# Kernel tuning notes

Measured on AMD Instinct MI355X. Metric: run time of the kernel, lower is better.

## Reference

```python
import jax, jax.numpy as jnp
import numpy as np
from math import comb

N_SEG = 100000      # number of Bezier segments
BEZ_ORDER = 3       # cubic Bezier -> 4 control points per segment
D = 3               # point dimension
BATCH, NPTS = 8, 1000000


def setup_inputs() -> dict:
    key = jax.random.key(0)
    k1, k2, k3 = jax.random.split(key, 3)
    # strictly ascending knot vector: cumsum of positive dx, starting at 0
    dx = jax.random.uniform(k1, (N_SEG,), dtype=jnp.float32, minval=0.5, maxval=1.5)
    x_knots = jnp.concatenate([jnp.zeros((1,), jnp.float32), jnp.cumsum(dx)])
    x_end = x_knots[-1]
    # eval points spread beyond [0, x_end) so the modulo wrap is exercised
    x_eval = jax.random.uniform(k2, (BATCH, NPTS), dtype=jnp.float32) * (2.0 * x_end) - 0.5 * x_end
    control_points = jax.random.normal(k3, (N_SEG, BEZ_ORDER + 1, D), dtype=jnp.float32)
    return {"x_knots": x_knots, "control_points": control_points, "x_eval": x_eval}


def _bernstein_basis(s, n):
    # s: [N] in [0,1] -> basis [N, n+1]; powers via cumprod (differentiable at s=0/1)
    binom = jnp.asarray([comb(n, k) for k in range(n + 1)], dtype=s.dtype)
    t = s[:, None]
    ones = jnp.ones_like(t)
    t_pow = jnp.cumprod(jnp.concatenate([ones, jnp.broadcast_to(t, (t.shape[0], n))], axis=1), axis=1)         # t^k
    u = 1.0 - t
    u_pow = jnp.cumprod(jnp.concatenate([ones, jnp.broadcast_to(u, (u.shape[0], n))], axis=1), axis=1)         # u^k
    return binom * t_pow * u_pow[:, ::-1]  # C(n,k) t^k (1-t)^(n-k)


def reference(x_knots, control_points, x_eval):
    n = control_points.shape[1] - 1
    d = control_points.shape[2]
    xstart = x_knots[:-1]                      # [n_seg]
    dx = x_knots[1:] - x_knots[:-1]            # [n_seg]
    # x_true = x_eval % xend  (Python modulo semantics, matches torch %)
    x_true = jnp.mod(x_eval.reshape(-1), x_knots[-1])        # [N]
    # bucket search: segment index such that xstart[i] <= x_true < xstart[i+1]
    idx = jnp.clip(jnp.searchsorted(xstart, x_true, side='right') - 1, 0, xstart.shape[0] - 1)
    s = (x_true - xstart[idx]) / dx[idx]                     # local param in [0,1)
    basis = _bernstein_basis(s, n)                           # [N, n+1]
    P = control_points[idx]                                  # gather: [N, n+1, d]
    vals = jnp.einsum('nk,nkd->nd', basis, P)                # [N, d]
    return vals.reshape(x_eval.shape + (d,)), idx.reshape(x_eval.shape)
```

## Files before the change

### kernel.cpp

```cpp
#include <hip/hip_runtime.h>
#include <hip/hip_fp16.h>
#include <math.h>

#define N_SEG 100000
#define LUT_BITS 18
#define LUT_SIZE (1 << LUT_BITS)
#define DELTA 0.03
#define PPT 4

using f32x4 = __attribute__((ext_vector_type(4))) float;
using u32x4 = __attribute__((ext_vector_type(4))) unsigned int;

#define LUT_OFF 0
#define REC_OFF (1 << 20)
#define WS_NEED (REC_OFF + (size_t)(N_SEG + 1) * 32)

__device__ __forceinline__ unsigned packh(float lo, float hi) {
    unsigned a = (unsigned)__half_as_ushort(__float2half(lo));
    unsigned b = (unsigned)__half_as_ushort(__float2half(hi));
    return a | (b << 16);
}
__device__ __forceinline__ float h2f(unsigned w, int hi) {
    return __half2float(__ushort_as_half((unsigned short)(hi ? (w >> 16) : (w & 0xFFFFu))));
}

__device__ __forceinline__ float mod_reduce(float x, float xe) {
    float r = x;
    r = (x >= xe) ? (x - xe) : r;
    r = (x < 0.0f) ? (x + xe) : r;
    return r;
}

__global__ void __launch_bounds__(256)
build_lut_kernel(const float* __restrict__ xk, unsigned* __restrict__ lut4) {
    int j = blockIdx.x * blockDim.x + threadIdx.x;
    if (j >= LUT_SIZE) return;
    double Wd = (double)xk[N_SEG] / (double)LUT_SIZE;
    double t = (double)j * Wd - DELTA;
    int lo = 0, hi = N_SEG;
    while (lo < hi) {
        int mid = (lo + hi) >> 1;
        if ((double)xk[mid] <= t) lo = mid + 1; else hi = mid;
    }
    int base = lo - 1;
    base = base < 0 ? 0 : (base > N_SEG - 1 ? N_SEG - 1 : base);
    lut4[j] = (unsigned)base;
}

__global__ void __launch_bounds__(256)
build_rec_kernel(const float* __restrict__ xk, const float* __restrict__ cp,
                 u32x4* __restrict__ rec) {
    int i = blockIdx.x * blockDim.x + threadIdx.x;
    if (i > N_SEG) return;
    if (i == N_SEG) {
        u32x4 w0 = { __float_as_uint(xk[N_SEG]), __float_as_uint(xk[N_SEG] + 1.0f), 0u, 0u };
        u32x4 w1 = { 0u, 0u, 0u, 0u };
        rec[2 * (size_t)i] = w0;
        rec[2 * (size_t)i + 1] = w1;
        return;
    }
    float x0 = xk[i];
    float x1 = xk[i + 1];
    const f32x4* p = reinterpret_cast<const f32x4*>(cp + (size_t)i * 12);
    f32x4 a0 = p[0], a1 = p[1], a2 = p[2];
    u32x4 w0 = { __float_as_uint(x0), __float_as_uint(x1),
                 packh(a0.x, a0.y), packh(a0.z, a0.w) };
    u32x4 w1 = { packh(a1.x, a1.y), packh(a1.z, a1.w),
                 packh(a2.x, a2.y), packh(a2.z, a2.w) };
    rec[2 * (size_t)i]     = w0;
    rec[2 * (size_t)i + 1] = w1;
}

__device__ __forceinline__ void blend_from_words(
        float r, int base, u32x4 A0, u32x4 A1, u32x4 B0, u32x4 B1,
        float* v, float* idxf) {
    float x0a = __uint_as_float(A0.x);
    float x1a = __uint_as_float(A0.y);
    int c = ((x1a <= r) && (base < N_SEG - 1)) ? 1 : 0;
    float x0 = c ? x1a : x0a;
    float x1 = c ? __uint_as_float(B0.y) : x1a;
    float s  = (r - x0) / (x1 - x0);

    unsigned cw0 = c ? B0.z : A0.z;
    unsigned cw1 = c ? B0.w : A0.w;
    unsigned cw2 = c ? B1.x : A1.x;
    unsigned cw3 = c ? B1.y : A1.y;
    unsigned cw4 = c ? B1.z : A1.z;
    unsigned cw5 = c ? B1.w : A1.w;

    float u = 1.0f - s;
    float s2 = s * s, u2 = u * u;
    float b0 = u2 * u;
    float b1 = (3.0f * s) * u2;
    float b2 = (3.0f * s2) * u;
    float b3 = s2 * s;

    float c0 = h2f(cw0, 0), c1  = h2f(cw0, 1);
    float c2 = h2f(cw1, 0), c3  = h2f(cw1, 1);
    float c4 = h2f(cw2, 0), c5  = h2f(cw2, 1);
    float c6 = h2f(cw3, 0), c7  = h2f(cw3, 1);
    float c8 = h2f(cw4, 0), c9  = h2f(cw4, 1);
    float c10 = h2f(cw5, 0), c11 = h2f(cw5, 1);

    v[0] = b0 * c0 + b1 * c3 + b2 * c6 + b3 * c9;
    v[1] = b0 * c1 + b1 * c4 + b2 * c7 + b3 * c10;
    v[2] = b0 * c2 + b1 * c5 + b2 * c8 + b3 * c11;
    *idxf = (float)(base + c);
}

__global__ void __launch_bounds__(256)
eval_kernel(const float* __restrict__ xk,
            const float* __restrict__ xev,
            float* __restrict__ out_vals,
            float* __restrict__ out_idx,
            const unsigned char* __restrict__ ws,
            int npts) {
    __shared__ u32x4 stage[4 * PPT * 4 * 64];
    unsigned char* stg = reinterpret_cast<unsigned char*>(stage);
    const unsigned* lut4 = reinterpret_cast<const unsigned*>(ws + LUT_OFF);
    const unsigned char* rec = ws + REC_OFF;

    int t = blockIdx.x * blockDim.x + threadIdx.x;
    int lane = threadIdx.x & 63;
    int wave = threadIdx.x >> 6;
    unsigned wbase = (unsigned)wave * (PPT * 4 * 1024);
    long i0 = (long)t * PPT;

    float xe = xk[N_SEG];
    float invW = (float)LUT_SIZE / xe;

    if (i0 + PPT - 1 < (long)npts) {
        f32x4 x4 = __builtin_nontemporal_load(reinterpret_cast<const f32x4*>(xev) + t);
        float r[PPT] = {x4.x, x4.y, x4.z, x4.w};
        #pragma unroll
        for (int q = 0; q < PPT; ++q) {
            r[q] = mod_reduce(r[q], xe);
            int j = (int)(r[q] * invW);
            j = j < 0 ? 0 : (j > LUT_SIZE - 1 ? LUT_SIZE - 1 : j);
            __builtin_amdgcn_global_load_lds(
                (const __attribute__((address_space(1))) void*)(lut4 + j),
                (__attribute__((address_space(3))) void*)(stg + wbase + q * 256 + lane * 4),
                4, 0, 0);
        }
        asm volatile("s_waitcnt vmcnt(0)" ::: "memory");
        __builtin_amdgcn_sched_barrier(0);

        int base[PPT];
        #pragma unroll
        for (int q = 0; q < PPT; ++q) {
            base[q] = *reinterpret_cast<volatile int*>(stg + wbase + q * 256 + lane * 4);
        }
        asm volatile("s_waitcnt lgkmcnt(0)" ::: "memory");
        __builtin_amdgcn_sched_barrier(0);

        #pragma unroll
        for (int q = 0; q < PPT; ++q) {
            const unsigned char* w = rec + (size_t)base[q] * 32;
            #pragma unroll
            for (int k = 0; k < 4; ++k) {
                __builtin_amdgcn_global_load_lds(
                    (const __attribute__((address_space(1))) void*)(w + 16 * k),
                    (__attribute__((address_space(3))) void*)(stg + wbase + (q * 4 + k) * 1024 + lane * 16),
                    16, 0, 0);
            }
        }
        asm volatile("s_waitcnt vmcnt(0)" ::: "memory");
        __builtin_amdgcn_sched_barrier(0);

        float vals[PPT * 3];
        float idxf[PPT];
        #pragma unroll
        for (int q = 0; q < PPT; ++q) {
            const u32x4* pl = reinterpret_cast<const u32x4*>(stg + wbase + q * 4096 + lane * 16);
            u32x4 A0 = pl[0];
            u32x4 A1 = pl[64];
            u32x4 B0 = pl[128];
            u32x4 B1 = pl[192];
            blend_from_words(r[q], base[q], A0, A1, B0, B1, &vals[q * 3], &idxf[q]);
        }
        f32x4* ov = reinterpret_cast<f32x4*>(out_vals + (size_t)t * 12);
        #pragma unroll
        for (int q = 0; q < 3; ++q) {
            f32x4 o = {vals[4 * q], vals[4 * q + 1], vals[4 * q + 2], vals[4 * q + 3]};
            ov[q] = o;
        }
        f32x4 oi = {idxf[0], idxf[1], idxf[2], idxf[3]};
        reinterpret_cast<f32x4*>(out_idx)[t] = oi;
    } else {
        for (long i = i0; i < (long)npts && i < i0 + PPT; ++i) {
            float r = mod_reduce(xev[i], xe);
            int j = (int)(r * invW);
            j = j < 0 ? 0 : (j > LUT_SIZE - 1 ? LUT_SIZE - 1 : j);
            int base = (int)lut4[j];
            const u32x4* w = reinterpret_cast<const u32x4*>(rec + (size_t)base * 32);
            u32x4 A0 = w[0], A1 = w[1], B0 = w[2], B1 = w[3];
            float v[3], idxv;
            blend_from_words(r, base, A0, A1, B0, B1, v, &idxv);
            out_vals[(size_t)i * 3 + 0] = v[0];
            out_vals[(size_t)i * 3 + 1] = v[1];
            out_vals[(size_t)i * 3 + 2] = v[2];
            out_idx[i] = idxv;
        }
    }
}

__global__ void __launch_bounds__(256)
eval_kernel_bs(const float* __restrict__ xk,
               const float* __restrict__ cp,
               const float* __restrict__ xev,
               float* __restrict__ out_vals,
               float* __restrict__ out_idx,
               int npts) {
    int i = blockIdx.x * blockDim.x + threadIdx.x;
    if (i >= npts) return;
    float xe = xk[N_SEG];
    float r = mod_reduce(xev[i], xe);
    int lo = 0, hi = N_SEG;
    while (lo < hi) {
        int mid = (lo + hi) >> 1;
        if (xk[mid] <= r) lo = mid + 1; else hi = mid;
    }
    int idx = lo - 1;
    if (idx < 0) idx = 0;
    float x0 = xk[idx];
    float s = (r - x0) / (xk[idx + 1] - x0);
    float u = 1.0f - s;
    float s2 = s * s, u2 = u * u;
    float b0 = u2 * u, b1f = (3.0f * s) * u2, b2f = (3.0f * s2) * u, b3f = s2 * s;
    const f32x4* p = reinterpret_cast<const f32x4*>(cp + (size_t)idx * 12);
    f32x4 pA = p[0], pB = p[1], pC = p[2];
    out_vals[(size_t)i * 3 + 0] = b0 * pA.x + b1f * pA.w + b2f * pB.z + b3f * pC.y;
    out_vals[(size_t)i * 3 + 1] = b0 * pA.y + b1f * pB.x + b2f * pB.w + b3f * pC.z;
    out_vals[(size_t)i * 3 + 2] = b0 * pA.z + b1f * pB.y + b2f * pC.x + b3f * pC.w;
    out_idx[i] = (float)idx;
}

extern "C" void kernel_launch(void* const* d_in, const int* in_sizes, int n_in,
                              void* d_out, int out_size, void* d_ws, size_t ws_size,
                              hipStream_t stream) {
    const float* xk  = (const float*)d_in[0];
    const float* cp  = (const float*)d_in[1];
    const float* xev = (const float*)d_in[2];
    int npts = in_sizes[2];

    float* out_vals = (float*)d_out;
    float* out_idx  = out_vals + (size_t)npts * 3;

    if (ws_size >= WS_NEED) {
        unsigned char* ws = (unsigned char*)d_ws;
        unsigned* lut4 = (unsigned*)(ws + LUT_OFF);
        u32x4*   rec   = (u32x4*)(ws + REC_OFF);
        build_lut_kernel<<<(LUT_SIZE + 255) / 256, 256, 0, stream>>>(xk, lut4);
        build_rec_kernel<<<(N_SEG + 1 + 255) / 256, 256, 0, stream>>>(xk, cp, rec);
        long nthreads = ((long)npts + PPT - 1) / PPT;
        int nblocks = (int)((nthreads + 255) / 256);
        eval_kernel<<<nblocks, 256, 0, stream>>>(xk, xev, out_vals, out_idx, ws, npts);
    } else {
        int nblocks = (npts + 255) / 256;
        eval_kernel_bs<<<nblocks, 256, 0, stream>>>(xk, cp, xev, out_vals, out_idx, npts);
    }
}
```

Before: 172.7 us.

## Store next-knot boundary in LUT entry to resolve segment before record fetch

Each LUT entry now holds the base segment plus the next knot position (8 bytes instead of 4). The kernel picks the exact segment from the LUT before fetching the record, so it loads only one 32-byte record per point instead of two. The LUT load also becomes a plain register load rather than an LDS-staged one. This halves the dependent gather traffic and the LDS staging footprint, at the cost of a LUT twice as large.

```diff
diff --git a/kernel.cpp b/kernel.cpp
--- a/kernel.cpp
+++ b/kernel.cpp
@@ -12,8 +12,8 @@
 using u32x4 = __attribute__((ext_vector_type(4))) unsigned int;
 
 #define LUT_OFF 0
-#define REC_OFF (1 << 20)
-#define WS_NEED (REC_OFF + (size_t)(N_SEG + 1) * 32)
+#define REC_OFF (2 << 20)
+#define WS_NEED (REC_OFF + (size_t)N_SEG * 32)
 
 __device__ __forceinline__ unsigned packh(float lo, float hi) {
     unsigned a = (unsigned)__half_as_ushort(__float2half(lo));
@@ -32,7 +32,7 @@
 }
 
 __global__ void __launch_bounds__(256)
-build_lut_kernel(const float* __restrict__ xk, unsigned* __restrict__ lut4) {
+build_lut_kernel(const float* __restrict__ xk, int2* __restrict__ lut8) {
     int j = blockIdx.x * blockDim.x + threadIdx.x;
     if (j >= LUT_SIZE) return;
     double Wd = (double)xk[N_SEG] / (double)LUT_SIZE;
@@ -44,21 +44,18 @@
     }
     int base = lo - 1;
     base = base < 0 ? 0 : (base > N_SEG - 1 ? N_SEG - 1 : base);
-    lut4[j] = (unsigned)base;
+    int2 e;
+    e.x = base;
+    e.y = (base + 1 <= N_SEG - 1) ? __float_as_int(xk[base + 1])
+                                  : __float_as_int(__builtin_inff());
+    lut8[j] = e;
 }
 
 __global__ void __launch_bounds__(256)
 build_rec_kernel(const float* __restrict__ xk, const float* __restrict__ cp,
                  u32x4* __restrict__ rec) {
     int i = blockIdx.x * blockDim.x + threadIdx.x;
-    if (i > N_SEG) return;
-    if (i == N_SEG) {
-        u32x4 w0 = { __float_as_uint(xk[N_SEG]), __float_as_uint(xk[N_SEG] + 1.0f), 0u, 0u };
-        u32x4 w1 = { 0u, 0u, 0u, 0u };
-        rec[2 * (size_t)i] = w0;
-        rec[2 * (size_t)i + 1] = w1;
-        return;
-    }
+    if (i >= N_SEG) return;
     float x0 = xk[i];
     float x1 = xk[i + 1];
     const f32x4* p = reinterpret_cast<const f32x4*>(cp + (size_t)i * 12);
@@ -71,22 +68,11 @@
     rec[2 * (size_t)i + 1] = w1;
 }
 
-__device__ __forceinline__ void blend_from_words(
-        float r, int base, u32x4 A0, u32x4 A1, u32x4 B0, u32x4 B1,
-        float* v, float* idxf) {
-    float x0a = __uint_as_float(A0.x);
-    float x1a = __uint_as_float(A0.y);
-    int c = ((x1a <= r) && (base < N_SEG - 1)) ? 1 : 0;
-    float x0 = c ? x1a : x0a;
-    float x1 = c ? __uint_as_float(B0.y) : x1a;
+__device__ __forceinline__ void blend_sel(float r, u32x4 A0, u32x4 A1,
+                                          float* v) {
+    float x0 = __uint_as_float(A0.x);
+    float x1 = __uint_as_float(A0.y);
     float s  = (r - x0) / (x1 - x0);
-
-    unsigned cw0 = c ? B0.z : A0.z;
-    unsigned cw1 = c ? B0.w : A0.w;
-    unsigned cw2 = c ? B1.x : A1.x;
-    unsigned cw3 = c ? B1.y : A1.y;
-    unsigned cw4 = c ? B1.z : A1.z;
-    unsigned cw5 = c ? B1.w : A1.w;
 
     float u = 1.0f - s;
     float s2 = s * s, u2 = u * u;
@@ -95,17 +81,16 @@
     float b2 = (3.0f * s2) * u;
     float b3 = s2 * s;
 
-    float c0 = h2f(cw0, 0), c1  = h2f(cw0, 1);
-    float c2 = h2f(cw1, 0), c3  = h2f(cw1, 1);
-    float c4 = h2f(cw2, 0), c5  = h2f(cw2, 1);
-    float c6 = h2f(cw3, 0), c7  = h2f(cw3, 1);
-    float c8 = h2f(cw4, 0), c9  = h2f(cw4, 1);
-    float c10 = h2f(cw5, 0), c11 = h2f(cw5, 1);
+    float c0 = h2f(A0.z, 0), c1  = h2f(A0.z, 1);
+    float c2 = h2f(A0.w, 0), c3  = h2f(A0.w, 1);
+    float c4 = h2f(A1.x, 0), c5  = h2f(A1.x, 1);
+    float c6 = h2f(A1.y, 0), c7  = h2f(A1.y, 1);
+    float c8 = h2f(A1.z, 0), c9  = h2f(A1.z, 1);
+    float c10 = h2f(A1.w, 0), c11 = h2f(A1.w, 1);
 
     v[0] = b0 * c0 + b1 * c3 + b2 * c6 + b3 * c9;
     v[1] = b0 * c1 + b1 * c4 + b2 * c7 + b3 * c10;
     v[2] = b0 * c2 + b1 * c5 + b2 * c8 + b3 * c11;
-    *idxf = (float)(base + c);
 }
 
 __global__ void __launch_bounds__(256)
@@ -115,15 +100,15 @@
             float* __restrict__ out_idx,
             const unsigned char* __restrict__ ws,
             int npts) {
-    __shared__ u32x4 stage[4 * PPT * 4 * 64];
+    __shared__ u32x4 stage[4 * PPT * 2 * 64];
     unsigned char* stg = reinterpret_cast<unsigned char*>(stage);
-    const unsigned* lut4 = reinterpret_cast<const unsigned*>(ws + LUT_OFF);
+    const int2* lut8 = reinterpret_cast<const int2*>(ws + LUT_OFF);
     const unsigned char* rec = ws + REC_OFF;
 
     int t = blockIdx.x * blockDim.x + threadIdx.x;
     int lane = threadIdx.x & 63;
     int wave = threadIdx.x >> 6;
-    unsigned wbase = (unsigned)wave * (PPT * 4 * 1024);
+    unsigned wbase = (unsigned)wave * (PPT * 2 * 1024);
     long i0 = (long)t * PPT;
 
     float xe = xk[N_SEG];
@@ -132,51 +117,42 @@
     if (i0 + PPT - 1 < (long)npts) {
         f32x4 x4 = __builtin_nontemporal_load(reinterpret_cast<const f32x4*>(xev) + t);
         float r[PPT] = {x4.x, x4.y, x4.z, x4.w};
+
+        int2 e[PPT];
         #pragma unroll
         for (int q = 0; q < PPT; ++q) {
             r[q] = mod_reduce(r[q], xe);
             int j = (int)(r[q] * invW);
             j = j < 0 ? 0 : (j > LUT_SIZE - 1 ? LUT_SIZE - 1 : j);
-            __builtin_amdgcn_global_load_lds(
-                (const __attribute__((address_space(1))) void*)(lut4 + j),
-                (__attribute__((address_space(3))) void*)(stg + wbase + q * 256 + lane * 4),
-                4, 0, 0);
+            e[q] = lut8[j];
+        }
+        __builtin_amdgcn_sched_barrier(0);
+
+        int idx[PPT];
+        #pragma unroll
+        for (int q = 0; q < PPT; ++q) {
+            idx[q] = e[q].x + ((__int_as_float(e[q].y) <= r[q]) ? 1 : 0);
+            const unsigned char* w = rec + (size_t)idx[q] * 32;
+            #pragma unroll
+            for (int k = 0; k < 2; ++k) {
+                __builtin_amdgcn_global_load_lds(
+                    (const __attribute__((address_space(1))) void*)(w + 16 * k),
+                    (__attribute__((address_space(3))) void*)(stg + wbase + (q * 2 + k) * 1024 + lane * 16),
+                    16, 0, 0);
+            }
         }
         asm volatile("s_waitcnt vmcnt(0)" ::: "memory");
         __builtin_amdgcn_sched_barrier(0);
 
-        int base[PPT];
-        #pragma unroll
-        for (int q = 0; q < PPT; ++q) {
-            base[q] = *reinterpret_cast<volatile int*>(stg + wbase + q * 256 + lane * 4);
-        }
-        asm volatile("s_waitcnt lgkmcnt(0)" ::: "memory");
-        __builtin_amdgcn_sched_barrier(0);
-
-        #pragma unroll
-        for (int q = 0; q < PPT; ++q) {
-            const unsigned char* w = rec + (size_t)base[q] * 32;
-            #pragma unroll
-            for (int k = 0; k < 4; ++k) {
-                __builtin_amdgcn_global_load_lds(
-                    (const __attribute__((address_space(1))) void*)(w + 16 * k),
-                    (__attribute__((address_space(3))) void*)(stg + wbase + (q * 4 + k) * 1024 + lane * 16),
-                    16, 0, 0);
-            }
-        }
-        asm volatile("s_waitcnt vmcnt(0)" ::: "memory");
-        __builtin_amdgcn_sched_barrier(0);
-
         float vals[PPT * 3];
         float idxf[PPT];
         #pragma unroll
         for (int q = 0; q < PPT; ++q) {
-            const u32x4* pl = reinterpret_cast<const u32x4*>(stg + wbase + q * 4096 + lane * 16);
+            const u32x4* pl = reinterpret_cast<const u32x4*>(stg + wbase + q * 2048 + lane * 16);
             u32x4 A0 = pl[0];
             u32x4 A1 = pl[64];
-            u32x4 B0 = pl[128];
-            u32x4 B1 = pl[192];
-            blend_from_words(r[q], base[q], A0, A1, B0, B1, &vals[q * 3], &idxf[q]);
+            blend_sel(r[q], A0, A1, &vals[q * 3]);
+            idxf[q] = (float)idx[q];
         }
         f32x4* ov = reinterpret_cast<f32x4*>(out_vals + (size_t)t * 12);
         #pragma unroll
@@ -191,15 +167,16 @@
             float r = mod_reduce(xev[i], xe);
             int j = (int)(r * invW);
             j = j < 0 ? 0 : (j > LUT_SIZE - 1 ? LUT_SIZE - 1 : j);
-            int base = (int)lut4[j];
-            const u32x4* w = reinterpret_cast<const u32x4*>(rec + (size_t)base * 32);
-            u32x4 A0 = w[0], A1 = w[1], B0 = w[2], B1 = w[3];
-            float v[3], idxv;
-            blend_from_words(r, base, A0, A1, B0, B1, v, &idxv);
+            int2 e = lut8[j];
+            int idx = e.x + ((__int_as_float(e.y) <= r) ? 1 : 0);
+            const u32x4* w = reinterpret_cast<const u32x4*>(rec + (size_t)idx * 32);
+            u32x4 A0 = w[0], A1 = w[1];
+            float v[3];
+            blend_sel(r, A0, A1, v);
             out_vals[(size_t)i * 3 + 0] = v[0];
             out_vals[(size_t)i * 3 + 1] = v[1];
             out_vals[(size_t)i * 3 + 2] = v[2];
-            out_idx[i] = idxv;
+            out_idx[i] = (float)idx;
         }
     }
 }
@@ -248,10 +225,10 @@
 
     if (ws_size >= WS_NEED) {
         unsigned char* ws = (unsigned char*)d_ws;
-        unsigned* lut4 = (unsigned*)(ws + LUT_OFF);
-        u32x4*   rec   = (u32x4*)(ws + REC_OFF);
-        build_lut_kernel<<<(LUT_SIZE + 255) / 256, 256, 0, stream>>>(xk, lut4);
-        build_rec_kernel<<<(N_SEG + 1 + 255) / 256, 256, 0, stream>>>(xk, cp, rec);
+        int2*  lut8 = (int2*)(ws + LUT_OFF);
+        u32x4* rec  = (u32x4*)(ws + REC_OFF);
+        build_lut_kernel<<<(LUT_SIZE + 255) / 256, 256, 0, stream>>>(xk, lut8);
+        build_rec_kernel<<<(N_SEG + 255) / 256, 256, 0, stream>>>(xk, cp, rec);
         long nthreads = ((long)npts + PPT - 1) / PPT;
         int nblocks = (int)((nthreads + 255) / 256);
         eval_kernel<<<nblocks, 256, 0, stream>>>(xk, xev, out_vals, out_idx, ws, npts);
```

New measurement: 161.0 us. 1.07x faster.

## Replace LDS-staged gathers with register gathers and double points per thread

Applied to the files above, without the earlier changes.

Removes the global_load_lds staging through shared memory for the LUT lookup and record gathers. The gathers now load straight into VGPRs, with asm pins and sched barriers keeping all loads issued before any use. Points per thread go from 4 to 8 to raise memory-level parallelism, and launch bounds ask for 4 blocks per CU. The cost is higher VGPR pressure (32 u32x4 values held in flight), which could cut occupancy or cause spills. The grid launch must also shrink to match PPT, and that part of the host code is not shown.

```diff
diff --git a/kernel.cpp b/kernel.cpp
--- a/kernel.cpp
+++ b/kernel.cpp
@@ -6,7 +6,7 @@
 #define LUT_BITS 18
 #define LUT_SIZE (1 << LUT_BITS)
 #define DELTA 0.03
-#define PPT 4
+#define PPT 8
 
 using f32x4 = __attribute__((ext_vector_type(4))) float;
 using u32x4 = __attribute__((ext_vector_type(4))) unsigned int;
@@ -14,6 +14,8 @@
 #define LUT_OFF 0
 #define REC_OFF (1 << 20)
 #define WS_NEED (REC_OFF + (size_t)(N_SEG + 1) * 32)
+
+#define PIN(x) asm volatile("" :: "v"(x))
 
 __device__ __forceinline__ unsigned packh(float lo, float hi) {
     unsigned a = (unsigned)__half_as_ushort(__float2half(lo));
@@ -55,7 +57,7 @@
     if (i == N_SEG) {
         u32x4 w0 = { __float_as_uint(xk[N_SEG]), __float_as_uint(xk[N_SEG] + 1.0f), 0u, 0u };
         u32x4 w1 = { 0u, 0u, 0u, 0u };
-        rec[2 * (size_t)i] = w0;
+        rec[2 * (size_t)i]     = w0;
         rec[2 * (size_t)i + 1] = w1;
         return;
     }
@@ -71,9 +73,9 @@
     rec[2 * (size_t)i + 1] = w1;
 }
 
-__device__ __forceinline__ void blend_from_words(
-        float r, int base, u32x4 A0, u32x4 A1, u32x4 B0, u32x4 B1,
-        float* v, float* idxf) {
+__device__ __forceinline__ void blend_window(float r, int base,
+                                             u32x4 A0, u32x4 A1, u32x4 B0, u32x4 B1,
+                                             float* v, float* idxf) {
     float x0a = __uint_as_float(A0.x);
     float x1a = __uint_as_float(A0.y);
     int c = ((x1a <= r) && (base < N_SEG - 1)) ? 1 : 0;
@@ -108,94 +110,83 @@
     *idxf = (float)(base + c);
 }
 
-__global__ void __launch_bounds__(256)
+__global__ void __launch_bounds__(256, 4)
 eval_kernel(const float* __restrict__ xk,
             const float* __restrict__ xev,
             float* __restrict__ out_vals,
             float* __restrict__ out_idx,
             const unsigned char* __restrict__ ws,
             int npts) {
-    __shared__ u32x4 stage[4 * PPT * 4 * 64];
-    unsigned char* stg = reinterpret_cast<unsigned char*>(stage);
     const unsigned* lut4 = reinterpret_cast<const unsigned*>(ws + LUT_OFF);
-    const unsigned char* rec = ws + REC_OFF;
+    const u32x4* rec = reinterpret_cast<const u32x4*>(ws + REC_OFF);
 
     int t = blockIdx.x * blockDim.x + threadIdx.x;
-    int lane = threadIdx.x & 63;
-    int wave = threadIdx.x >> 6;
-    unsigned wbase = (unsigned)wave * (PPT * 4 * 1024);
     long i0 = (long)t * PPT;
 
     float xe = xk[N_SEG];
     float invW = (float)LUT_SIZE / xe;
 
     if (i0 + PPT - 1 < (long)npts) {
-        f32x4 x4 = __builtin_nontemporal_load(reinterpret_cast<const f32x4*>(xev) + t);
-        float r[PPT] = {x4.x, x4.y, x4.z, x4.w};
+        f32x4 xa = __builtin_nontemporal_load(reinterpret_cast<const f32x4*>(xev) + 2 * t);
+        f32x4 xb = __builtin_nontemporal_load(reinterpret_cast<const f32x4*>(xev) + 2 * t + 1);
+        float r[PPT] = {xa.x, xa.y, xa.z, xa.w, xb.x, xb.y, xb.z, xb.w};
+        const unsigned* lp[PPT];
         #pragma unroll
         for (int q = 0; q < PPT; ++q) {
             r[q] = mod_reduce(r[q], xe);
             int j = (int)(r[q] * invW);
             j = j < 0 ? 0 : (j > LUT_SIZE - 1 ? LUT_SIZE - 1 : j);
-            __builtin_amdgcn_global_load_lds(
-                (const __attribute__((address_space(1))) void*)(lut4 + j),
-                (__attribute__((address_space(3))) void*)(stg + wbase + q * 256 + lane * 4),
-                4, 0, 0);
-        }
-        asm volatile("s_waitcnt vmcnt(0)" ::: "memory");
+            lp[q] = lut4 + j;
+        }
+        unsigned basew[PPT];
+        #pragma unroll
+        for (int q = 0; q < PPT; ++q) basew[q] = *lp[q];
         __builtin_amdgcn_sched_barrier(0);
-
-        int base[PPT];
-        #pragma unroll
-        for (int q = 0; q < PPT; ++q) {
-            base[q] = *reinterpret_cast<volatile int*>(stg + wbase + q * 256 + lane * 4);
-        }
-        asm volatile("s_waitcnt lgkmcnt(0)" ::: "memory");
+        #pragma unroll
+        for (int q = 0; q < PPT; ++q) PIN(basew[q]);
+
+        u32x4 A0[PPT], A1[PPT], B0[PPT], B1[PPT];
+        #pragma unroll
+        for (int q = 0; q < PPT; ++q) {
+            const u32x4* w = rec + 2 * (size_t)basew[q];
+            A0[q] = w[0];
+            A1[q] = w[1];
+            B0[q] = w[2];
+            B1[q] = w[3];
+        }
         __builtin_amdgcn_sched_barrier(0);
-
-        #pragma unroll
-        for (int q = 0; q < PPT; ++q) {
-            const unsigned char* w = rec + (size_t)base[q] * 32;
-            #pragma unroll
-            for (int k = 0; k < 4; ++k) {
-                __builtin_amdgcn_global_load_lds(
-                    (const __attribute__((address_space(1))) void*)(w + 16 * k),
-                    (__attribute__((address_space(3))) void*)(stg + wbase + (q * 4 + k) * 1024 + lane * 16),
-                    16, 0, 0);
-            }
-        }
-        asm volatile("s_waitcnt vmcnt(0)" ::: "memory");
-        __builtin_amdgcn_sched_barrier(0);
+        #pragma unroll
+        for (int q = 0; q < PPT; ++q) {
+            PIN(A0[q].x); PIN(A1[q].x); PIN(B0[q].x); PIN(B1[q].x);
+        }
 
         float vals[PPT * 3];
         float idxf[PPT];
         #pragma unroll
         for (int q = 0; q < PPT; ++q) {
-            const u32x4* pl = reinterpret_cast<const u32x4*>(stg + wbase + q * 4096 + lane * 16);
-            u32x4 A0 = pl[0];
-            u32x4 A1 = pl[64];
-            u32x4 B0 = pl[128];
-            u32x4 B1 = pl[192];
-            blend_from_words(r[q], base[q], A0, A1, B0, B1, &vals[q * 3], &idxf[q]);
-        }
-        f32x4* ov = reinterpret_cast<f32x4*>(out_vals + (size_t)t * 12);
-        #pragma unroll
-        for (int q = 0; q < 3; ++q) {
+            blend_window(r[q], (int)basew[q], A0[q], A1[q], B0[q], B1[q],
+                         &vals[q * 3], &idxf[q]);
+        }
+        f32x4* ov = reinterpret_cast<f32x4*>(out_vals + (size_t)t * (PPT * 3));
+        #pragma unroll
+        for (int q = 0; q < PPT * 3 / 4; ++q) {
             f32x4 o = {vals[4 * q], vals[4 * q + 1], vals[4 * q + 2], vals[4 * q + 3]};
             ov[q] = o;
         }
-        f32x4 oi = {idxf[0], idxf[1], idxf[2], idxf[3]};
-        reinterpret_cast<f32x4*>(out_idx)[t] = oi;
+        f32x4 oi0 = {idxf[0], idxf[1], idxf[2], idxf[3]};
+        f32x4 oi1 = {idxf[4], idxf[5], idxf[6], idxf[7]};
+        reinterpret_cast<f32x4*>(out_idx)[2 * t]     = oi0;
+        reinterpret_cast<f32x4*>(out_idx)[2 * t + 1] = oi1;
     } else {
         for (long i = i0; i < (long)npts && i < i0 + PPT; ++i) {
             float r = mod_reduce(xev[i], xe);
             int j = (int)(r * invW);
             j = j < 0 ? 0 : (j > LUT_SIZE - 1 ? LUT_SIZE - 1 : j);
             int base = (int)lut4[j];
-            const u32x4* w = reinterpret_cast<const u32x4*>(rec + (size_t)base * 32);
+            const u32x4* w = rec + 2 * (size_t)base;
             u32x4 A0 = w[0], A1 = w[1], B0 = w[2], B1 = w[3];
             float v[3], idxv;
-            blend_from_words(r, base, A0, A1, B0, B1, v, &idxv);
+            blend_window(r, base, A0, A1, B0, B1, v, &idxv);
             out_vals[(size_t)i * 3 + 0] = v[0];
             out_vals[(size_t)i * 3 + 1] = v[1];
             out_vals[(size_t)i * 3 + 2] = v[2];
```

New measurement: 270.5 us. 56.6% more time.
